# Kernel tuning notes

Hardware: AMD Instinct MI355X
Metric: run time of the kernel (lower is better)

The kernel has to match this reference:

```python
import jax, jax.numpy as jnp
import numpy as np

BETA = 0.904837
V_TH = 1.0
SURR_K = 25.0


def _spike(v):
    # Heaviside forward; surrogate gradient irrelevant for fwd-only.
    return (v >= V_TH).astype(v.dtype)


def setup_inputs() -> dict:
    key = jax.random.key(0)
    k1, k2 = jax.random.split(key)
    B, T, H = 16, 1024, 2048
    input_current = jax.random.normal(k1, (B, T, H), dtype=jnp.float32)
    v_init = jax.random.normal(k2, (B, H), dtype=jnp.float32)
    return {"input_current": input_current, "v_init": v_init}


def reference(input_current, v_init):
    # input_current: (B, T, H), v_init: (B, H)
    def step(carry, i_t):
        v, s_prev = carry
        v = BETA * v * (1.0 - s_prev) + i_t  # hard reset via (1 - s_prev)
        s = _spike(v)
        return (v, s), (s, v)

    s0 = jnp.zeros_like(v_init)
    # scan over time axis: move T to leading dim
    (v_final, _), (spikes_t, membrane_t) = jax.lax.scan(
        step, (v_init, s0), jnp.swapaxes(input_current, 0, 1)
    )
    spikes = jnp.swapaxes(spikes_t, 0, 1)      # (B, T, H)
    membrane = jnp.swapaxes(membrane_t, 0, 1)  # (B, T, H)
    return spikes, membrane, v_final
```

## Files before the change

### kernel.cpp

```cpp
#include <hip/hip_runtime.h>


constexpr int B_  = 16;
constexpr int T_  = 1024;
constexpr int H_  = 2048;
constexpr float BETA = 0.904837f;

constexpr int C   = 16;
constexpr int NCH = T_ / C;
constexpr int OPS = (C * 64) / (64 * 4);

__device__ __forceinline__ void async_copy16(const void* g, void* s) {
    __builtin_amdgcn_global_load_lds(
        (const __attribute__((address_space(1))) void*)g,
        (__attribute__((address_space(3))) void*)s,
        16, 0, 0);
}

__global__ __launch_bounds__(64) void lif_fwd_kernel(
    const float* __restrict__ in,
    const float* __restrict__ v0,
    float* __restrict__ sp,
    float* __restrict__ mem,
    float* __restrict__ vf)
{
    __shared__ float lds_buf[4][C * 64];

    const int lane = threadIdx.x;
    const int w    = blockIdx.x;
    const int b    = w >> 5;
    const int col  = (w & 31) * 64;

    const size_t seq = (size_t)b * T_ * H_ + col;

    const char* sbase = (const char*)(in + seq)
                      + (size_t)(lane >> 4) * (H_ * 4)
                      + (size_t)(lane & 15) * 16;

    float* __restrict__ spp = sp  + seq + lane;
    float* __restrict__ mpp = mem + seq + lane;

    const int vidx = b * H_ + col + lane;
    float v = v0[vidx];
    float s = 0.0f;

    auto stage = [&](int c) {
        const char* gb = sbase + (size_t)c * C * (H_ * 4);
#pragma unroll
        for (int p = 0; p < OPS; ++p)
            async_copy16(gb + (size_t)(4 * p) * (H_ * 4),
                         &lds_buf[c & 3][p * 256]);
    };

    stage(0); stage(1); stage(2);
    asm volatile("s_waitcnt vmcnt(8)" ::: "memory");

    for (int c = 0; c < NCH; ++c) {
        const float* lbuf = lds_buf[c & 3];
        const size_t obase = (size_t)c * C * H_;
#pragma unroll
        for (int t = 0; t < C; ++t) {
            const float x = lbuf[t * 64 + lane];

            v = BETA * v * (1.0f - s) + x;
            s = (v >= 1.0f) ? 1.0f : 0.0f;

            const size_t o = obase + (size_t)t * H_;
            __builtin_nontemporal_store(s, spp + o);
            __builtin_nontemporal_store(v, mpp + o);
        }

        if (c + 3 < NCH) stage(c + 3);

        if (c + 3 < NCH)       asm volatile("s_waitcnt vmcnt(40)" ::: "memory");
        else if (c + 2 < NCH)  asm volatile("s_waitcnt vmcnt(36)" ::: "memory");
        else if (c + 1 < NCH)  asm volatile("s_waitcnt vmcnt(32)" ::: "memory");
    }

    vf[vidx] = v;
}

extern "C" void kernel_launch(void* const* d_in, const int* in_sizes, int n_in,
                              void* d_out, int out_size, void* d_ws, size_t ws_size,
                              hipStream_t stream) {
    const float* in = (const float*)d_in[0];
    const float* v0 = (const float*)d_in[1];

    float* out = (float*)d_out;
    const size_t n_bth = (size_t)B_ * T_ * H_;
    float* sp  = out;
    float* mem = out + n_bth;
    float* vf  = out + 2 * n_bth;

    const int grid = B_ * (H_ / 64);
    lif_fwd_kernel<<<grid, 64, 0, stream>>>(in, v0, sp, mem, vf);
}
```

Before: 365.7 us.

## Stage outputs through LDS and write them as 16-byte vector stores

Each chunk's spike and membrane results now go into LDS and are then written back as 16-byte nontemporal float4 stores, replacing 32 scalar 4-byte stores per lane per chunk. The prefetch of chunk c+3 now issues before the compute rather than after, and the vmcnt wait thresholds are recomputed for the new mix of loads and stores. The aim is fewer, wider store instructions and an earlier load issue, which should reduce memory-instruction pressure in this bandwidth-bound kernel. The cost is extra LDS traffic and a read-after-write hazard: the code has no barrier, so correctness relies on the block being a single wavefront, and the hand-tuned wait counts are fragile.

New measurement: 379.3 us. 1.04x slower.

```diff
diff --git a/kernel.cpp b/kernel.cpp
--- a/kernel.cpp
+++ b/kernel.cpp
@@ -9,6 +9,9 @@
 constexpr int C   = 16;
 constexpr int NCH = T_ / C;
 constexpr int OPS = (C * 64) / (64 * 4);
+constexpr int G4  = C / 4;
+
+typedef __attribute__((ext_vector_type(4))) float fx4;
 
 __device__ __forceinline__ void async_copy16(const void* g, void* s) {
     __builtin_amdgcn_global_load_lds(
@@ -24,7 +27,9 @@
     float* __restrict__ mem,
     float* __restrict__ vf)
 {
-    __shared__ float lds_buf[4][C * 64];
+    __shared__ float lds_in[4][C * 64];
+    __shared__ float lds_s[C * 64];
+    __shared__ float lds_v[C * 64];
 
     const int lane = threadIdx.x;
     const int w    = blockIdx.x;
@@ -33,12 +38,11 @@
 
     const size_t seq = (size_t)b * T_ * H_ + col;
 
-    const char* sbase = (const char*)(in + seq)
-                      + (size_t)(lane >> 4) * (H_ * 4)
-                      + (size_t)(lane & 15) * 16;
+    const size_t row4 = (size_t)(lane >> 4) * H_ + (size_t)(lane & 15) * 4;
+    const char* sbase = (const char*)(in + seq) + row4 * 4;
 
-    float* __restrict__ spp = sp  + seq + lane;
-    float* __restrict__ mpp = mem + seq + lane;
+    float* __restrict__ spp = sp  + seq + row4;
+    float* __restrict__ mpp = mem + seq + row4;
 
     const int vidx = b * H_ + col + lane;
     float v = v0[vidx];
@@ -49,15 +53,16 @@
 #pragma unroll
         for (int p = 0; p < OPS; ++p)
             async_copy16(gb + (size_t)(4 * p) * (H_ * 4),
-                         &lds_buf[c & 3][p * 256]);
+                         &lds_in[c & 3][p * 256]);
     };
 
     stage(0); stage(1); stage(2);
     asm volatile("s_waitcnt vmcnt(8)" ::: "memory");
 
     for (int c = 0; c < NCH; ++c) {
-        const float* lbuf = lds_buf[c & 3];
-        const size_t obase = (size_t)c * C * H_;
+        if (c + 3 < NCH) stage(c + 3);
+
+        const float* lbuf = lds_in[c & 3];
 #pragma unroll
         for (int t = 0; t < C; ++t) {
             const float x = lbuf[t * 64 + lane];
@@ -65,16 +70,30 @@
             v = BETA * v * (1.0f - s) + x;
             s = (v >= 1.0f) ? 1.0f : 0.0f;
 
-            const size_t o = obase + (size_t)t * H_;
-            __builtin_nontemporal_store(s, spp + o);
-            __builtin_nontemporal_store(v, mpp + o);
+            lds_s[t * 64 + lane] = s;
+            lds_v[t * 64 + lane] = v;
         }
 
-        if (c + 3 < NCH) stage(c + 3);
+        {
+            const size_t ob = (size_t)c * C * H_;
+#pragma unroll
+            for (int g = 0; g < G4; ++g) {
+                const int lidx = (g * 4 + (lane >> 4)) * 64 + (lane & 15) * 4;
+                const fx4 vs = *(const fx4*)&lds_s[lidx];
+                const fx4 vv = *(const fx4*)&lds_v[lidx];
+                const size_t o = ob + (size_t)(g * 4) * H_;
+                __builtin_nontemporal_store(vs, (fx4*)(spp + o));
+                __builtin_nontemporal_store(vv, (fx4*)(mpp + o));
+            }
+        }
 
-        if (c + 3 < NCH)       asm volatile("s_waitcnt vmcnt(40)" ::: "memory");
-        else if (c + 2 < NCH)  asm volatile("s_waitcnt vmcnt(36)" ::: "memory");
-        else if (c + 1 < NCH)  asm volatile("s_waitcnt vmcnt(32)" ::: "memory");
+        if (c + 1 < NCH) {
+            if (c == 0)            asm volatile("s_waitcnt vmcnt(16)" ::: "memory");
+            else if (c == 1)       asm volatile("s_waitcnt vmcnt(24)" ::: "memory");
+            else if (c + 3 < NCH)  asm volatile("s_waitcnt vmcnt(32)" ::: "memory");
+            else if (c + 3 == NCH) asm volatile("s_waitcnt vmcnt(28)" ::: "memory");
+            else                   asm volatile("s_waitcnt vmcnt(24)" ::: "memory");
+        }
     }
 
     vf[vidx] = v;
```
